# Performance work log

Measured on AMD Instinct MI355X. Metric: run time of the kernel, lower is better.

The kernel has to match this reference:

```python
import jax, jax.numpy as jnp
import numpy as np

GROUPS = 32
GN_EPS = 1e-6
LN_EPS = 1e-5
HEADS = 8
DH = 40


def group_norm(x, w, b):
    # x: [B, C, H, W], GroupNorm over (C//GROUPS, H, W) within each group
    B, C, H, W = x.shape
    xg = x.reshape(B, GROUPS, C // GROUPS, H, W)
    mu = xg.mean(axis=(2, 3, 4), keepdims=True)
    var = xg.var(axis=(2, 3, 4), keepdims=True)
    xg = (xg - mu) * jax.lax.rsqrt(var + GN_EPS)
    return xg.reshape(B, C, H, W) * w[None, :, None, None] + b[None, :, None, None]


def layer_norm(x, w, b):
    mu = x.mean(axis=-1, keepdims=True)
    var = x.var(axis=-1, keepdims=True)
    return (x - mu) * jax.lax.rsqrt(var + LN_EPS) * w + b


def attention(x, ctx, wq, wk, wv, wo, bo):
    # x: [B, N, D], ctx: [B, M, Dc]; weights stored (in, out)
    B, N, _ = x.shape
    M = ctx.shape[1]
    q = (x @ wq).reshape(B, N, HEADS, DH)
    k = (ctx @ wk).reshape(B, M, HEADS, DH)
    v = (ctx @ wv).reshape(B, M, HEADS, DH)
    sim = jnp.einsum('bihd,bjhd->bhij', q, k) * (DH ** -0.5)
    attn = jax.nn.softmax(sim, axis=-1)
    out = jnp.einsum('bhij,bjhd->bihd', attn, v).reshape(B, N, HEADS * DH)
    return out @ wo + bo


def geglu_ff(x, w1, b1, w2, b2):
    h = x @ w1 + b1
    a, g = jnp.split(h, 2, axis=-1)
    return (a * jax.nn.gelu(g, approximate=False)) @ w2 + b2


def conv1x1(x, w, b):
    # w: [C_out, C_in]
    return jnp.einsum('bihw,oi->bohw', x, w) + b[None, :, None, None]


def reference(x, context, gn_w, gn_b, pin_w, pin_b,
              ln1_w, ln1_b, q1, k1, v1, o1_w, o1_b,
              ln2_w, ln2_b, q2, k2, v2, o2_w, o2_b,
              ln3_w, ln3_b, ff1_w, ff1_b, ff2_w, ff2_b,
              pout_w, pout_b):
    B, C, H, W = x.shape
    x_in = x
    h = group_norm(x, gn_w, gn_b)
    h = conv1x1(h, pin_w, pin_b)
    h = h.reshape(B, C, H * W).transpose(0, 2, 1)  # b (h w) c
    # BasicTransformerBlock
    h = attention(layer_norm(h, ln1_w, ln1_b), layer_norm(h, ln1_w, ln1_b), q1, k1, v1, o1_w, o1_b) + h
    h = attention(layer_norm(h, ln2_w, ln2_b), context, q2, k2, v2, o2_w, o2_b) + h
    h = geglu_ff(layer_norm(h, ln3_w, ln3_b), ff1_w, ff1_b, ff2_w, ff2_b) + h
    h = h.transpose(0, 2, 1).reshape(B, C, H, W)
    h = conv1x1(h, pout_w, pout_b)
    return h + x_in


def setup_inputs() -> dict:
    key = jax.random.key(0)
    ks = jax.random.split(key, 20)
    B, C, H, W = 1, 320, 64, 64
    CTX_N, CTX_D = 77, 768
    INNER, FFI = 320, 1280

    def n(k, shape, s=0.02):
        return jax.random.normal(k, shape, jnp.float32) * s

    return {
        'x': jax.random.normal(ks[0], (B, C, H, W), jnp.float32),
        'context': jax.random.normal(ks[1], (B, CTX_N, CTX_D), jnp.float32),
        'gn_w': jnp.ones((C,), jnp.float32), 'gn_b': jnp.zeros((C,), jnp.float32),
        'pin_w': n(ks[2], (INNER, C)), 'pin_b': jnp.zeros((INNER,), jnp.float32),
        'ln1_w': jnp.ones((INNER,), jnp.float32), 'ln1_b': jnp.zeros((INNER,), jnp.float32),
        'q1': n(ks[3], (INNER, INNER)), 'k1': n(ks[4], (INNER, INNER)), 'v1': n(ks[5], (INNER, INNER)),
        'o1_w': n(ks[6], (INNER, INNER)), 'o1_b': jnp.zeros((INNER,), jnp.float32),
        'ln2_w': jnp.ones((INNER,), jnp.float32), 'ln2_b': jnp.zeros((INNER,), jnp.float32),
        'q2': n(ks[7], (INNER, INNER)), 'k2': n(ks[8], (CTX_D, INNER)), 'v2': n(ks[9], (CTX_D, INNER)),
        'o2_w': n(ks[10], (INNER, INNER)), 'o2_b': jnp.zeros((INNER,), jnp.float32),
        'ln3_w': jnp.ones((INNER,), jnp.float32), 'ln3_b': jnp.zeros((INNER,), jnp.float32),
        'ff1_w': n(ks[11], (INNER, 2 * FFI)), 'ff1_b': jnp.zeros((2 * FFI,), jnp.float32),
        'ff2_w': n(ks[12], (FFI, INNER)), 'ff2_b': jnp.zeros((INNER,), jnp.float32),
        'pout_w': n(ks[13], (C, INNER)), 'pout_b': jnp.zeros((C,), jnp.float32),
    }
```

## Files before the change

kernel.cpp:

```cpp
#include <hip/hip_runtime.h>
#include <hip/hip_bf16.h>
#include <math.h>

#define N_SEQ  4096
#define DMODEL 320
#define NHEADS 8
#define DHEAD  40
#define CTXN   77
#define CTXD   768
#define FFI    1280

typedef short s8v __attribute__((ext_vector_type(8)));
typedef short s4v __attribute__((ext_vector_type(4)));
typedef float f4v __attribute__((ext_vector_type(4)));
typedef unsigned short u16;

static __device__ __forceinline__ u16 bf16u(float x) {
    unsigned u = __float_as_uint(x);
    return (u16)((u + 0x7FFFu + ((u >> 16) & 1u)) >> 16);
}
static __device__ __forceinline__ float b2f(u16 v) { return __uint_as_float((unsigned)v << 16); }
static __device__ __forceinline__ unsigned pack2(float a, float b) {
    return (unsigned)bf16u(a) | ((unsigned)bf16u(b) << 16);
}

struct WC { const float* s; u16* d; int K, O, trans; };
struct WCs { WC a[12]; };
__global__ __launch_bounds__(256) void wcast2_k(WCs P) {
    __shared__ float tile[32][33];
    WC w = P.a[blockIdx.y];
    if (w.trans) {
        int ntk = w.K >> 5, nto = w.O >> 5;
        int tid = blockIdx.x;
        if (tid >= ntk * nto) return;
        int tk = tid % ntk, to = tid / ntk;
        int lr = threadIdx.x >> 5, lc = threadIdx.x & 31;
#pragma unroll
        for (int p = 0; p < 4; ++p) {
            int k = tk * 32 + p * 8 + lr;
            tile[p * 8 + lr][lc] = w.s[(size_t)k * w.O + to * 32 + lc];
        }
        __syncthreads();
#pragma unroll
        for (int p = 0; p < 4; ++p) {
            int o = to * 32 + p * 8 + lr;
            w.d[(size_t)o * w.K + tk * 32 + lc] = bf16u(tile[lc][p * 8 + lr]);
        }
    } else {
        int nel = w.K * w.O;
        for (int e = blockIdx.x * 256 + threadIdx.x; e < nel; e += gridDim.x * 256)
            w.d[e] = bf16u(w.s[e]);
    }
}

__global__ __launch_bounds__(256) void gn_stats_k(const float* __restrict__ x,
                                                  const float* __restrict__ gw, const float* __restrict__ gb,
                                                  float* __restrict__ sc, float* __restrict__ sh) {
    __shared__ float red[512];
    __shared__ float ms[2];
    int g = blockIdx.x, t = threadIdx.x;
    const float* xp = x + (size_t)g * 40960;
    float s = 0.f, ss = 0.f;
    for (int i = t; i < 40960; i += 256) { float v = xp[i]; s += v; ss += v * v; }
    red[t] = s; red[256 + t] = ss;
    __syncthreads();
    for (int st = 128; st > 0; st >>= 1) {
        if (t < st) { red[t] += red[t + st]; red[256 + t] += red[256 + t + st]; }
        __syncthreads();
    }
    if (t == 0) {
        float mean = red[0] / 40960.f;
        float var  = red[256] / 40960.f - mean * mean;
        ms[0] = mean; ms[1] = rsqrtf(var + 1e-6f);
    }
    __syncthreads();
    if (t < 10) {
        int c = g * 10 + t;
        float scv = gw[c] * ms[1];
        sc[c] = scv;
        sh[c] = gb[c] - ms[0] * scv;
    }
}

__global__ __launch_bounds__(256) void ln_stats_k(const float* __restrict__ in,
                                                  float* __restrict__ mu, float* __restrict__ rs) {
    int row = blockIdx.x * 4 + (threadIdx.x >> 6), l = threadIdx.x & 63;
    const float* p = in + (size_t)row * DMODEL;
    float s = 0.f, ss = 0.f;
#pragma unroll
    for (int j = 0; j < 5; ++j) { float v = p[l + 64 * j]; s += v; ss += v * v; }
    for (int o = 32; o > 0; o >>= 1) { s += __shfl_xor(s, o); ss += __shfl_xor(ss, o); }
    if (l == 0) {
        float mean = s * (1.f / 320.f);
        float var  = ss * (1.f / 320.f) - mean * mean;
        mu[row] = mean;
        rs[row] = rsqrtf(var + 1e-5f);
    }
}

struct GArg { const u16* Wt; const float* bias; float* outf; u16* outb; int ob_mode; };
#define GP 72
#define QSCALE 0.22811012f

template<int SITE>
__global__ __launch_bounds__(256) void gemm_t(const void* __restrict__ Av, int a_mode, int lda,
                                              const float* __restrict__ mu, const float* __restrict__ rs,
                                              const float* __restrict__ cw, const float* __restrict__ cb,
                                              GArg g0, GArg g1, GArg g2,
                                              const float* __restrict__ res,
                                              int Mrows, int K, int Oout, int obT_stride) {
    __shared__ __align__(16) u16 As[2][64 * GP];
    __shared__ __align__(16) u16 Wsm[2][64 * GP];
    const int t = threadIdx.x;
    const int w = t >> 6, lane = t & 63, c = lane & 15, quad = lane >> 4;
    const int o0 = blockIdx.x * 64, n0 = blockIdx.y * 64;
    GArg g = (blockIdx.z == 0) ? g0 : ((blockIdx.z == 1) ? g1 : g2);
    const f4v zero = {0.f, 0.f, 0.f, 0.f};
    f4v acc[4] = {zero, zero, zero, zero};
    const s8v z8 = {0, 0, 0, 0, 0, 0, 0, 0};
    const int nk = K >> 6;

    float fA[16];
    s8v bA0 = z8, bA1 = z8;
    s8v wv0, wv1;

    auto loadW = [&](int k0) {
        int i0 = t, i1 = t + 256;
        wv0 = *(const s8v*)(g.Wt + (size_t)(o0 + (i0 >> 3)) * K + k0 + (i0 & 7) * 8);
        wv1 = *(const s8v*)(g.Wt + (size_t)(o0 + (i1 >> 3)) * K + k0 + (i1 & 7) * 8);
    };
    auto storeW = [&](int b) {
        int i0 = t, i1 = t + 256;
        *(s8v*)&Wsm[b][(i0 >> 3) * GP + (i0 & 7) * 8] = wv0;
        *(s8v*)&Wsm[b][(i1 >> 3) * GP + (i1 & 7) * 8] = wv1;
    };
    auto loadA = [&](int k0) {
        if (a_mode == 0) {
            const u16* A = (const u16*)Av;
            int i0 = t, i1 = t + 256;
            int nA = n0 + (i0 >> 3), nB = n0 + (i1 >> 3);
            bA0 = (nA < Mrows) ? *(const s8v*)(A + (size_t)nA * lda + k0 + (i0 & 7) * 8) : z8;
            bA1 = (nB < Mrows) ? *(const s8v*)(A + (size_t)nB * lda + k0 + (i1 & 7) * 8) : z8;
        } else if (a_mode == 1) {
            const float* A = (const float*)Av;
            int r = t >> 2, s16 = (t & 3) * 16;
            int n = n0 + r;
            if (n < Mrows) {
                const float* src = A + (size_t)n * lda + k0 + s16;
#pragma unroll
                for (int i = 0; i < 16; ++i) fA[i] = src[i];
            } else {
#pragma unroll
                for (int i = 0; i < 16; ++i) fA[i] = 0.f;
            }
        } else if (a_mode == 2) {
            const float* A = (const float*)Av;
#pragma unroll
            for (int j = 0; j < 16; ++j) {
                int e = t + 256 * j; int nn = e & 63, kk = e >> 6;
                int n = n0 + nn, kgl = k0 + kk;
                fA[j] = (n < Mrows) ? A[(size_t)kgl * lda + n] * cw[kgl] + cb[kgl] : 0.f;
            }
        } else if (a_mode == 3) {
            const float* A = (const float*)Av;
            int r = t >> 2, s16 = (t & 3) * 16;
            int n = n0 + r;
            if (n < Mrows) {
                const float* src = A + (size_t)n * lda + k0 + s16;
                const float* cwp = cw + k0 + s16;
                const float* cbp = cb + k0 + s16;
                float m_ = mu[n], rr = rs[n];
#pragma unroll
                for (int i = 0; i < 16; ++i) fA[i] = (src[i] - m_) * rr * cwp[i] + cbp[i];
            } else {
#pragma unroll
                for (int i = 0; i < 16; ++i) fA[i] = 0.f;
            }
        } else {
            const u16* Op = (const u16*)Av;
            const float* lp = mu;
            int r = t >> 2, s16 = (t & 3) * 16;
            int n = n0 + r;
            int ch0 = k0 + s16;
            int hdA = ch0 / 40;
            int hdB = (ch0 + 15) / 40;
            float invA = 1.f / (lp[(size_t)hdA * N_SEQ + n] + lp[(size_t)(8 + hdA) * N_SEQ + n]);
            float invB = (hdB == hdA) ? invA
                       : 1.f / (lp[(size_t)hdB * N_SEQ + n] + lp[(size_t)(8 + hdB) * N_SEQ + n]);
#pragma unroll
            for (int i = 0; i < 16; ++i) {
                int ch = ch0 + i;
                int hd = ch / 40;
                int d  = ch - hd * 40;
                float num = b2f(Op[((size_t)hd * N_SEQ + n) * DHEAD + d])
                          + b2f(Op[((size_t)(8 + hd) * N_SEQ + n) * DHEAD + d]);
                fA[i] = num * ((hd == hdA) ? invA : invB);
            }
        }
    };
    auto storeA = [&](int b) {
        if (a_mode == 0) {
            int i0 = t, i1 = t + 256;
            *(s8v*)&As[b][(i0 >> 3) * GP + (i0 & 7) * 8] = bA0;
            *(s8v*)&As[b][(i1 >> 3) * GP + (i1 & 7) * 8] = bA1;
        } else if (a_mode == 2) {
#pragma unroll
            for (int j = 0; j < 16; ++j) {
                int e = t + 256 * j; int nn = e & 63, kk = e >> 6;
                As[b][nn * GP + kk] = bf16u(fA[j]);
            }
        } else {
            int r = t >> 2, s16 = (t & 3) * 16;
            unsigned* dst = (unsigned*)&As[b][r * GP + s16];
#pragma unroll
            for (int i = 0; i < 8; ++i) dst[i] = pack2(fA[2 * i], fA[2 * i + 1]);
        }
    };

    loadA(0); loadW(0);
    storeA(0); storeW(0);
    __syncthreads();
    for (int k = 0; k < nk; ++k) {
        const int cur = k & 1;
        if (k + 1 < nk) { loadA((k + 1) << 6); loadW((k + 1) << 6); }
        s8v a0 = *(const s8v*)&As[cur][(w * 16 + c) * GP + quad * 8];
        s8v a1 = *(const s8v*)&As[cur][(w * 16 + c) * GP + 32 + quad * 8];
#pragma unroll
        for (int nt = 0; nt < 4; ++nt) {
            s8v b0 = *(const s8v*)&Wsm[cur][(nt * 16 + c) * GP + quad * 8];
            s8v b1 = *(const s8v*)&Wsm[cur][(nt * 16 + c) * GP + 32 + quad * 8];
            acc[nt] = __builtin_amdgcn_mfma_f32_16x16x32_bf16(a0, b0, acc[nt], 0, 0, 0);
            acc[nt] = __builtin_amdgcn_mfma_f32_16x16x32_bf16(a1, b1, acc[nt], 0, 0, 0);
        }
        if (k + 1 < nk) { storeA(1 - cur); storeW(1 - cur); }
        __syncthreads();
    }
#pragma unroll
    for (int nt = 0; nt < 4; ++nt) {
        int o = o0 + nt * 16 + c;
        float vv[4];
#pragma unroll
        for (int r = 0; r < 4; ++r) vv[r] = acc[nt][r] + (g.bias ? g.bias[o] : 0.f);
        if (g.ob_mode == 3) {
            int nb = n0 + w * 16 + quad * 4;
            const float4 x4 = *(const float4*)(res + (size_t)o * obT_stride + nb);
            float4 o4 = make_float4(vv[0] + x4.x, vv[1] + x4.y, vv[2] + x4.z, vv[3] + x4.w);
            *(float4*)(g.outf + (size_t)o * obT_stride + nb) = o4;
        } else if (g.ob_mode == 4) {
#pragma unroll
            for (int r = 0; r < 4; ++r) {
                int n = n0 + w * 16 + quad * 4 + r;
                float vvv = vv[r];
                if (o < 320) vvv *= QSCALE;
                u16 bv = bf16u(vvv);
                if (o < 320)      g0.outb[(size_t)n * 320 + o] = bv;
                else if (o < 640) g1.outb[(size_t)n * 320 + (o - 320)] = bv;
                else              g2.outb[(size_t)(o - 640) * obT_stride + n] = bv;
            }
        } else {
#pragma unroll
            for (int r = 0; r < 4; ++r) {
                int n = n0 + w * 16 + quad * 4 + r;
                if (n >= Mrows) continue;
                float v = vv[r];
                if (res) v += res[(size_t)n * Oout + o];
                if (g.outf) g.outf[(size_t)n * Oout + o] = v;
                if (g.ob_mode == 1) g.outb[(size_t)n * Oout + o] = bf16u(v);
                else if (g.ob_mode == 2) g.outb[(size_t)o * obT_stride + n] = bf16u(v);
            }
        }
    }
}

__global__ __launch_bounds__(256) void gemm_gg(const float* __restrict__ A, int lda,
                                               const float* __restrict__ mu, const float* __restrict__ rs,
                                               const float* __restrict__ cw, const float* __restrict__ cb,
                                               const u16* __restrict__ Wt, const float* __restrict__ bias,
                                               u16* __restrict__ outb,
                                               int K, int Oout, int geglu_off) {
    __shared__ __align__(16) u16 As[64 * GP];
    __shared__ __align__(16) u16 Wsm[64 * GP];
    __shared__ __align__(16) u16 Wgm[64 * GP];
    const int t = threadIdx.x;
    const int w = t >> 6, lane = t & 63, c = lane & 15, quad = lane >> 4;
    const int o0 = blockIdx.x * 64, n0 = blockIdx.y * 64;
    const f4v zero = {0.f, 0.f, 0.f, 0.f};
    f4v acc[4]  = {zero, zero, zero, zero};
    f4v accg[4] = {zero, zero, zero, zero};
    const int nk = K >> 6;

    float fA[16];
    s8v wv0, wv1, gv0, gv1;

    auto loadWG = [&](int k0) {
        int i0 = t, i1 = t + 256;
        wv0 = *(const s8v*)(Wt + (size_t)(o0 + (i0 >> 3)) * K + k0 + (i0 & 7) * 8);
        wv1 = *(const s8v*)(Wt + (size_t)(o0 + (i1 >> 3)) * K + k0 + (i1 & 7) * 8);
        gv0 = *(const s8v*)(Wt + (size_t)(o0 + (i0 >> 3) + geglu_off) * K + k0 + (i0 & 7) * 8);
        gv1 = *(const s8v*)(Wt + (size_t)(o0 + (i1 >> 3) + geglu_off) * K + k0 + (i1 & 7) * 8);
    };
    auto storeWG = [&]() {
        int i0 = t, i1 = t + 256;
        *(s8v*)&Wsm[(i0 >> 3) * GP + (i0 & 7) * 8] = wv0;
        *(s8v*)&Wsm[(i1 >> 3) * GP + (i1 & 7) * 8] = wv1;
        *(s8v*)&Wgm[(i0 >> 3) * GP + (i0 & 7) * 8] = gv0;
        *(s8v*)&Wgm[(i1 >> 3) * GP + (i1 & 7) * 8] = gv1;
    };
    auto loadA = [&](int k0) {
        int r = t >> 2, s16 = (t & 3) * 16;
        int n = n0 + r;
        const float* src = A + (size_t)n * lda + k0 + s16;
        const float* cwp = cw + k0 + s16;
        const float* cbp = cb + k0 + s16;
        float m_ = mu[n], rr = rs[n];
#pragma unroll
        for (int i = 0; i < 16; ++i) fA[i] = (src[i] - m_) * rr * cwp[i] + cbp[i];
    };
    auto storeA = [&]() {
        int r = t >> 2, s16 = (t & 3) * 16;
        unsigned* dst = (unsigned*)&As[r * GP + s16];
#pragma unroll
        for (int i = 0; i < 8; ++i) dst[i] = pack2(fA[2 * i], fA[2 * i + 1]);
    };

    loadA(0); loadWG(0);
    storeA(); storeWG();
    __syncthreads();
    for (int k = 0; k < nk; ++k) {
        if (k + 1 < nk) { loadA((k + 1) << 6); loadWG((k + 1) << 6); }
        s8v a0 = *(const s8v*)&As[(w * 16 + c) * GP + quad * 8];
        s8v a1 = *(const s8v*)&As[(w * 16 + c) * GP + 32 + quad * 8];
#pragma unroll
        for (int nt = 0; nt < 4; ++nt) {
            s8v b0 = *(const s8v*)&Wsm[(nt * 16 + c) * GP + quad * 8];
            s8v b1 = *(const s8v*)&Wsm[(nt * 16 + c) * GP + 32 + quad * 8];
            acc[nt] = __builtin_amdgcn_mfma_f32_16x16x32_bf16(a0, b0, acc[nt], 0, 0, 0);
            acc[nt] = __builtin_amdgcn_mfma_f32_16x16x32_bf16(a1, b1, acc[nt], 0, 0, 0);
            s8v q0 = *(const s8v*)&Wgm[(nt * 16 + c) * GP + quad * 8];
            s8v q1 = *(const s8v*)&Wgm[(nt * 16 + c) * GP + 32 + quad * 8];
            accg[nt] = __builtin_amdgcn_mfma_f32_16x16x32_bf16(a0, q0, accg[nt], 0, 0, 0);
            accg[nt] = __builtin_amdgcn_mfma_f32_16x16x32_bf16(a1, q1, accg[nt], 0, 0, 0);
        }
        __syncthreads();
        if (k + 1 < nk) {
            storeA(); storeWG();
            __syncthreads();
        }
    }
#pragma unroll
    for (int nt = 0; nt < 4; ++nt) {
        int o = o0 + nt * 16 + c;
#pragma unroll
        for (int r = 0; r < 4; ++r) {
            int n = n0 + w * 16 + quad * 4 + r;
            float v = acc[nt][r] + bias[o];
            float gg = accg[nt][r] + bias[o + geglu_off];
            v = v * 0.5f * gg * (1.f + erff(gg * 0.70710678118654752f));
            outb[(size_t)n * Oout + o] = bf16u(v);
        }
    }
}

#define KSP 40
#define PSP 140
#define VP  136
__global__ __launch_bounds__(256) void attn_self8_k(const u16* __restrict__ qb, const u16* __restrict__ kb,
                                                    const u16* __restrict__ vt,
                                                    u16* __restrict__ Opart, float* __restrict__ lpart) {
    __shared__ __align__(16) u16 Ks[128 * KSP];
    __shared__ __align__(16) u16 Ps[64 * PSP];
    __shared__ __align__(16) u16 Vs[48 * VP];
    const int t = threadIdx.x;
    const int w = t >> 6, lane = t & 63, c = lane & 15, quad = lane >> 4;
    const int hd = blockIdx.y, ks = blockIdx.z;
    const int q0 = blockIdx.x * 64;
    const f4v zero = {0.f, 0.f, 0.f, 0.f};
    const s8v z8 = {0, 0, 0, 0, 0, 0, 0, 0};

    for (int i = t; i < 8 * VP / 2; i += 256) ((unsigned*)&Vs[40 * VP])[i] = 0u;
    __syncthreads();
    if (t < VP) Vs[40 * VP + t] = (u16)0x3F80;

    const u16* qrow = qb + (size_t)(q0 + w * 16 + c) * DMODEL + hd * DHEAD;
    s8v qa0 = *(const s8v*)(qrow + quad * 8);
    s8v qa1 = z8;
    if (quad == 0) qa1 = *(const s8v*)(qrow + 32);

    const int i0 = t, i1 = t + 256, i2 = t + 512;
    const int r0 = i0 / 5, s0 = i0 - r0 * 5;
    const int r1 = i1 / 5, s1 = i1 - r1 * 5;
    const int r2 = i2 / 5, s2 = i2 - r2 * 5;
    const u16* kq0 = kb + (size_t)(ks * 2048 + r0) * DMODEL + hd * DHEAD + s0 * 8;
    const u16* kq1 = kb + (size_t)(ks * 2048 + r1) * DMODEL + hd * DHEAD + s1 * 8;
    const u16* kq2 = kb + (size_t)(ks * 2048 + (t < 128 ? r2 : r0)) * DMODEL + hd * DHEAD + (t < 128 ? s2 : s0) * 8;
    u16* ksd0 = &Ks[r0 * KSP + s0 * 8];
    u16* ksd1 = &Ks[r1 * KSP + s1 * 8];
    u16* ksd2 = &Ks[(t < 128 ? r2 : r0) * KSP + (t < 128 ? s2 : s0) * 8];
    const int d0 = i0 >> 4, g0v = i0 & 15;
    const int d1 = i1 >> 4, g1v = i1 & 15;
    const int d2 = (t < 128 ? (i2 >> 4) : d0), g2v = (t < 128 ? (i2 & 15) : g0v);
    const u16* vq0 = vt + (size_t)(hd * DHEAD + d0) * N_SEQ + ks * 2048 + g0v * 8;
    const u16* vq1 = vt + (size_t)(hd * DHEAD + d1) * N_SEQ + ks * 2048 + g1v * 8;
    const u16* vq2 = vt + (size_t)(hd * DHEAD + d2) * N_SEQ + ks * 2048 + g2v * 8;
    u16* vsd0 = &Vs[d0 * VP + g0v * 8];
    u16* vsd1 = &Vs[d1 * VP + g1v * 8];
    u16* vsd2 = &Vs[d2 * VP + g2v * 8];
    const size_t kadv = (size_t)128 * DMODEL;

    s8v kA = *(const s8v*)kq0, kB = *(const s8v*)kq1, kC = *(const s8v*)kq2;
    s8v vA = *(const s8v*)vq0, vB = *(const s8v*)vq1, vC = *(const s8v*)vq2;
    kq0 += kadv; kq1 += kadv; kq2 += kadv;
    vq0 += 128;  vq1 += 128;  vq2 += 128;

    f4v o0 = zero, o1 = zero, o2 = zero;

    for (int kt = 0; kt < 16; ++kt) {
        __syncthreads();
        *(s8v*)ksd0 = kA; *(s8v*)ksd1 = kB;
        *(s8v*)vsd0 = vA; *(s8v*)vsd1 = vB;
        if (t < 128) { *(s8v*)ksd2 = kC; *(s8v*)vsd2 = vC; }
        if (kt + 1 < 16) {
            kA = *(const s8v*)kq0; kB = *(const s8v*)kq1;
            vA = *(const s8v*)vq0; vB = *(const s8v*)vq1;
            if (t < 128) { kC = *(const s8v*)kq2; vC = *(const s8v*)vq2; }
            kq0 += kadv; kq1 += kadv; kq2 += kadv;
            vq0 += 128;  vq1 += 128;  vq2 += 128;
        }
        __syncthreads();

        f4v sarr[8];
#pragma unroll
        for (int nt = 0; nt < 8; ++nt) {
            const int kr = nt * 16 + c;
            s8v b0 = *(const s8v*)&Ks[kr * KSP + quad * 8];
            s8v b1 = z8;
            if (quad == 0) b1 = *(const s8v*)&Ks[kr * KSP + 32];
            f4v s = __builtin_amdgcn_mfma_f32_16x16x32_bf16(qa0, b0, zero, 0, 0, 0);
            s = __builtin_amdgcn_mfma_f32_16x16x32_bf16(qa1, b1, s, 0, 0, 0);
            sarr[nt] = s;
        }

        u16* psw = &Ps[(size_t)(w * 16 + quad * 4) * PSP + c];
#pragma unroll
        for (int reg = 0; reg < 8; ++reg) {
            const int colb = (reg >> 2) * 64 + (reg & 3) * 16;
#pragma unroll
            for (int r = 0; r < 4; ++r) {
                float pv = exp2f(sarr[reg][r]);
                psw[r * PSP + colb] = (u16)(__float_as_uint(pv) >> 16);
            }
        }

        const u16* prow = &Ps[(size_t)(w * 16 + c) * PSP];
#pragma unroll
        for (int h2 = 0; h2 < 2; ++h2) {
            s8v pa0, pa1;
            {
                s4v lo = *(const s4v*)(prow + h2 * 64 + quad * 8);
                s4v hi = *(const s4v*)(prow + h2 * 64 + quad * 8 + 4);
                pa0 = (s8v){lo[0], lo[1], lo[2], lo[3], hi[0], hi[1], hi[2], hi[3]};
                s4v lo2 = *(const s4v*)(prow + h2 * 64 + 32 + quad * 8);
                s4v hi2 = *(const s4v*)(prow + h2 * 64 + 32 + quad * 8 + 4);
                pa1 = (s8v){lo2[0], lo2[1], lo2[2], lo2[3], hi2[0], hi2[1], hi2[2], hi2[3]};
            }
            {
                s8v v0 = *(const s8v*)&Vs[(0 * 16 + c) * VP + h2 * 64 + quad * 8];
                s8v v1 = *(const s8v*)&Vs[(0 * 16 + c) * VP + h2 * 64 + 32 + quad * 8];
                o0 = __builtin_amdgcn_mfma_f32_16x16x32_bf16(pa0, v0, o0, 0, 0, 0);
                o0 = __builtin_amdgcn_mfma_f32_16x16x32_bf16(pa1, v1, o0, 0, 0, 0);
            }
            {
                s8v v0 = *(const s8v*)&Vs[(1 * 16 + c) * VP + h2 * 64 + quad * 8];
                s8v v1 = *(const s8v*)&Vs[(1 * 16 + c) * VP + h2 * 64 + 32 + quad * 8];
                o1 = __builtin_amdgcn_mfma_f32_16x16x32_bf16(pa0, v0, o1, 0, 0, 0);
                o1 = __builtin_amdgcn_mfma_f32_16x16x32_bf16(pa1, v1, o1, 0, 0, 0);
            }
            {
                s8v v0 = *(const s8v*)&Vs[(2 * 16 + c) * VP + h2 * 64 + quad * 8];
                s8v v1 = *(const s8v*)&Vs[(2 * 16 + c) * VP + h2 * 64 + 32 + quad * 8];
                o2 = __builtin_amdgcn_mfma_f32_16x16x32_bf16(pa0, v0, o2, 0, 0, 0);
                o2 = __builtin_amdgcn_mfma_f32_16x16x32_bf16(pa1, v1, o2, 0, 0, 0);
            }
        }
    }

    const size_t pb = (size_t)(ks * 8 + hd) * N_SEQ;
#pragma unroll
    for (int r = 0; r < 4; ++r) {
        int q = q0 + w * 16 + quad * 4 + r;
        u16* op = Opart + (pb + q) * DHEAD;
        op[c]      = bf16u(o0[r]);
        op[16 + c] = bf16u(o1[r]);
        if (c < 8) op[32 + c] = bf16u(o2[r]);
        if (c == 8) lpart[pb + q] = o2[r];
    }
}

__global__ __launch_bounds__(256) void attn_cross3_k(const u16* __restrict__ qb,
                                                     const u16* __restrict__ kb,
                                                     const u16* __restrict__ vt,
                                                     u16* __restrict__ outb) {
    __shared__ __align__(16) u16 KsPs[64 * PSP];
    __shared__ __align__(16) u16 Vs[48 * VP];
    const int t = threadIdx.x;
    const int w = t >> 6, lane = t & 63, c = lane & 15, quad = lane >> 4;
    const int hd = blockIdx.y;
    const int q0 = blockIdx.x * 64;
    const float SC2 = 0.15811388300841897f * 1.4426950408889634f;
    const f4v zero = {0.f, 0.f, 0.f, 0.f};
    const s8v z8 = {0, 0, 0, 0, 0, 0, 0, 0};

    for (int i = t; i < 48 * VP / 2; i += 256) ((unsigned*)Vs)[i] = 0u;
    __syncthreads();
    if (t < VP) Vs[40 * VP + t] = (u16)0x3F80;
    for (int i = t; i < 400; i += 256) {
        int d = i / 10, kc = i - d * 10;
        s8v v = *(const s8v*)(vt + (size_t)(hd * DHEAD + d) * 128 + kc * 8);
        if (kc == 9) { v[5] = 0; v[6] = 0; v[7] = 0; }
        *(s8v*)&Vs[d * VP + kc * 8] = v;
    }
    for (int i = t; i < 385; i += 256) {
        int r = i / 5, sg = i - r * 5;
        *(s8v*)&KsPs[r * KSP + sg * 8] = *(const s8v*)(kb + (size_t)r * DMODEL + hd * DHEAD + sg * 8);
    }
    const u16* qrow = qb + (size_t)(q0 + w * 16 + c) * DMODEL + hd * DHEAD;
    s8v qa0 = *(const s8v*)(qrow + quad * 8);
    s8v qa1 = z8;
    if (quad == 0) qa1 = *(const s8v*)(qrow + 32);
    __syncthreads();

    f4v sarr[5];
#pragma unroll
    for (int nt = 0; nt < 5; ++nt) {
        const int kr = nt * 16 + c;
        s8v b0 = *(const s8v*)&KsPs[kr * KSP + quad * 8];
        s8v b1 = z8;
        if (quad == 0) b1 = *(const s8v*)&KsPs[kr * KSP + 32];
        f4v s = __builtin_amdgcn_mfma_f32_16x16x32_bf16(qa0, b0, zero, 0, 0, 0);
        s = __builtin_amdgcn_mfma_f32_16x16x32_bf16(qa1, b1, s, 0, 0, 0);
        sarr[nt] = s;
    }
    __syncthreads();

    u16* psw = &KsPs[(size_t)(w * 16 + quad * 4) * PSP + c];
#pragma unroll
    for (int r = 0; r < 4; ++r) {
        float s4 = (c < 13) ? sarr[4][r] : -1e30f;
        float mx = fmaxf(fmaxf(fmaxf(sarr[0][r], sarr[1][r]), fmaxf(sarr[2][r], sarr[3][r])), s4);
        mx = fmaxf(mx, __shfl_xor(mx, 1));
        mx = fmaxf(mx, __shfl_xor(mx, 2));
        mx = fmaxf(mx, __shfl_xor(mx, 4));
        mx = fmaxf(mx, __shfl_xor(mx, 8));
#pragma unroll
        for (int nt = 0; nt < 4; ++nt)
            psw[r * PSP + nt * 16] = bf16u(exp2f((sarr[nt][r] - mx) * SC2));
        psw[r * PSP + 64] = (c < 13) ? bf16u(exp2f((s4 - mx) * SC2)) : (u16)0;
        psw[r * PSP + 80] = 0;
    }

    const u16* prow = &KsPs[(size_t)(w * 16 + c) * PSP];
    f4v o0 = zero, o1 = zero, o2 = zero;
#pragma unroll
    for (int ch = 0; ch < 3; ++ch) {
        s4v lo = *(const s4v*)(prow + ch * 32 + quad * 8);
        s4v hi = *(const s4v*)(prow + ch * 32 + quad * 8 + 4);
        s8v pa = (s8v){lo[0], lo[1], lo[2], lo[3], hi[0], hi[1], hi[2], hi[3]};
        s8v v0 = *(const s8v*)&Vs[(0 * 16 + c) * VP + ch * 32 + quad * 8];
        o0 = __builtin_amdgcn_mfma_f32_16x16x32_bf16(pa, v0, o0, 0, 0, 0);
        s8v v1 = *(const s8v*)&Vs[(1 * 16 + c) * VP + ch * 32 + quad * 8];
        o1 = __builtin_amdgcn_mfma_f32_16x16x32_bf16(pa, v1, o1, 0, 0, 0);
        s8v v2 = *(const s8v*)&Vs[(2 * 16 + c) * VP + ch * 32 + quad * 8];
        o2 = __builtin_amdgcn_mfma_f32_16x16x32_bf16(pa, v2, o2, 0, 0, 0);
    }

#pragma unroll
    for (int r = 0; r < 4; ++r) {
        float inv = 1.f / __shfl(o2[r], (lane & 48) | 8);
        int q = q0 + w * 16 + quad * 4 + r;
        u16* op = outb + (size_t)q * DMODEL + hd * DHEAD;
        op[c]      = bf16u(o0[r] * inv);
        op[16 + c] = bf16u(o1[r] * inv);
        if (c < 8) op[32 + c] = bf16u(o2[r] * inv);
    }
}

extern "C" void kernel_launch(void* const* d_in, const int* in_sizes, int n_in,
                              void* d_out, int out_size, void* d_ws, size_t ws_size,
                              hipStream_t stream) {
    const float* x      = (const float*)d_in[0];
    const float* ctx    = (const float*)d_in[1];
    const float* gn_w   = (const float*)d_in[2];
    const float* gn_b   = (const float*)d_in[3];
    const float* pin_w  = (const float*)d_in[4];
    const float* pin_b  = (const float*)d_in[5];
    const float* ln1_w  = (const float*)d_in[6];
    const float* ln1_b  = (const float*)d_in[7];
    const float* q1     = (const float*)d_in[8];
    const float* k1     = (const float*)d_in[9];
    const float* v1     = (const float*)d_in[10];
    const float* o1_w   = (const float*)d_in[11];
    const float* o1_b   = (const float*)d_in[12];
    const float* ln2_w  = (const float*)d_in[13];
    const float* ln2_b  = (const float*)d_in[14];
    const float* q2     = (const float*)d_in[15];
    const float* k2     = (const float*)d_in[16];
    const float* v2     = (const float*)d_in[17];
    const float* o2_w   = (const float*)d_in[18];
    const float* o2_b   = (const float*)d_in[19];
    const float* ln3_w  = (const float*)d_in[20];
    const float* ln3_b  = (const float*)d_in[21];
    const float* ff1_w  = (const float*)d_in[22];
    const float* ff1_b  = (const float*)d_in[23];
    const float* ff2_w  = (const float*)d_in[24];
    const float* ff2_b  = (const float*)d_in[25];
    const float* pout_w = (const float*)d_in[26];
    const float* pout_b = (const float*)d_in[27];
    float* out = (float*)d_out;

    char* base = (char*)d_ws;
    float* h     = (float*)(base);
    u16*   qb16  = (u16*)(base + 5242880);
    u16*   kb16  = (u16*)(base + 7864320);
    u16*   vt16  = (u16*)(base + 10485760);
    u16*   ao16  = (u16*)(base + 13107200);
    u16*   ffg16 = (u16*)(base + 5242880);
    u16*   wbase = (u16*)(base + 15728640);
    u16* pinT  = wbase;
    u16* q1T   = pinT  + 102400;
    u16* k1T   = q1T   + 102400;
    u16* v1T   = k1T   + 102400;
    u16* o1T   = v1T   + 102400;
    u16* q2T   = o1T   + 102400;
    u16* o2T   = q2T   + 102400;
    u16* k2T   = o2T   + 102400;
    u16* v2T   = k2T   + 245760;
    u16* ff1T  = v2T   + 245760;
    u16* ff2T  = ff1T  + 819200;
    u16* poutT = ff2T  + 409600;
    float* lnmu = (float*)(base + 20807680);
    float* lnrs = lnmu + 4096;
    u16*   k2b16 = (u16*)(lnrs + 4096);
    u16*   v2t16 = (u16*)(lnrs + 4096 + 25600);
    u16*   Opart = (u16*)(lnrs + 4096 + 51200);
    float* lpart = (float*)(Opart + (size_t)2 * 8 * 4096 * 40);
    float* gnsc  = lpart + 2 * 8 * 4096;
    float* gnsh  = gnsc + 320;

    WCs wd;
    wd.a[0]  = {pin_w,  pinT,  320,  320,  0};
    wd.a[1]  = {q1,     q1T,   320,  320,  1};
    wd.a[2]  = {k1,     k1T,   320,  320,  1};
    wd.a[3]  = {v1,     v1T,   320,  320,  1};
    wd.a[4]  = {o1_w,   o1T,   320,  320,  1};
    wd.a[5]  = {q2,     q2T,   320,  320,  1};
    wd.a[6]  = {o2_w,   o2T,   320,  320,  1};
    wd.a[7]  = {k2,     k2T,   768,  320,  1};
    wd.a[8]  = {v2,     v2T,   768,  320,  1};
    wd.a[9]  = {ff1_w,  ff1T,  320,  2560, 1};
    wd.a[10] = {ff2_w,  ff2T,  1280, 320,  1};
    wd.a[11] = {pout_w, poutT, 320,  320,  0};
    wcast2_k<<<dim3(800, 12), 256, 0, stream>>>(wd);

    GArg gz = {nullptr, nullptr, nullptr, nullptr, 0};

    gn_stats_k<<<32, 256, 0, stream>>>(x, gn_w, gn_b, gnsc, gnsh);
    {
        GArg g0 = {pinT, pin_b, h, nullptr, 0};
        gemm_t<0><<<dim3(5, 64, 1), 256, 0, stream>>>(x, 2, 4096, nullptr, nullptr, gnsc, gnsh,
                                                      g0, gz, gz, nullptr, 4096, 320, 320, 0);
    }
    ln_stats_k<<<1024, 256, 0, stream>>>(h, lnmu, lnrs);
    {
        GArg g0 = {q1T, nullptr, nullptr, qb16, 4};
        GArg g1 = {nullptr, nullptr, nullptr, kb16, 0};
        GArg g2 = {nullptr, nullptr, nullptr, vt16, 0};
        gemm_t<1><<<dim3(15, 64, 1), 256, 0, stream>>>(h, 3, 320, lnmu, lnrs, ln1_w, ln1_b,
                                                       g0, g1, g2, nullptr, 4096, 320, 960, 4096);
    }
    attn_self8_k<<<dim3(64, 8, 2), 256, 0, stream>>>(qb16, kb16, vt16, Opart, lpart);
    {
        GArg g0 = {o1T, o1_b, h, nullptr, 0};
        gemm_t<2><<<dim3(5, 64, 1), 256, 0, stream>>>(Opart, 4, 0, lpart, nullptr, nullptr, nullptr,
                                                      g0, gz, gz, h, 4096, 320, 320, 0);
    }
    ln_stats_k<<<1024, 256, 0, stream>>>(h, lnmu, lnrs);
    {
        GArg g0 = {q2T, nullptr, nullptr, qb16, 1};
        gemm_t<3><<<dim3(5, 64, 1), 256, 0, stream>>>(h, 3, 320, lnmu, lnrs, ln2_w, ln2_b,
                                                      g0, gz, gz, nullptr, 4096, 320, 320, 0);
    }
    {
        GArg g0 = {k2T, nullptr, nullptr, k2b16, 1};
        GArg g1 = {v2T, nullptr, nullptr, v2t16, 2};
        gemm_t<4><<<dim3(5, 2, 2), 256, 0, stream>>>(ctx, 1, 768, nullptr, nullptr, nullptr, nullptr,
                                                     g0, g1, gz, nullptr, 77, 768, 320, 128);
    }
    attn_cross3_k<<<dim3(64, 8), 256, 0, stream>>>(qb16, k2b16, v2t16, ao16);
    {
        GArg g0 = {o2T, o2_b, h, nullptr, 0};
        gemm_t<5><<<dim3(5, 64, 1), 256, 0, stream>>>(ao16, 0, 320, nullptr, nullptr, nullptr, nullptr,
                                                      g0, gz, gz, h, 4096, 320, 320, 0);
    }
    ln_stats_k<<<1024, 256, 0, stream>>>(h, lnmu, lnrs);
    gemm_gg<<<dim3(20, 64, 1), 256, 0, stream>>>(h, 320, lnmu, lnrs, ln3_w, ln3_b,
                                                 ff1T, ff1_b, ffg16, 320, 1280, 1280);
    {
        GArg g0 = {ff2T, ff2_b, h, nullptr, 0};
        gemm_t<6><<<dim3(5, 64, 1), 256, 0, stream>>>(ffg16, 0, 1280, nullptr, nullptr, nullptr, nullptr,
                                                      g0, gz, gz, h, 4096, 1280, 320, 0);
    }
    {
        GArg g0 = {poutT, pout_b, out, nullptr, 3};
        gemm_t<7><<<dim3(5, 64, 1), 256, 0, stream>>>(h, 1, 320, nullptr, nullptr, nullptr, nullptr,
                                                      g0, gz, gz, x, 4096, 320, 320, 4096);
    }
}
```

Before: 439.3 us.

## Load GEMM weight tiles directly into LDS with XOR-swizzled layout

Weight tiles in the templated GEMM now move from global memory straight into shared memory using the global_load_lds builtin. This replaces the path of loading into registers and then storing to LDS. Because that load cannot pad rows, the tile drops its padded stride and uses an XOR swizzle on the 16-byte chunk index to avoid bank conflicts on reads. The aim is to save VGPRs and LDS-store instructions, and to overlap weight fetch with the MFMA work. The risk is a correctness error in the swizzle mapping or in the async-load wait semantics before the __syncthreads.

```diff
diff --git a/kernel.cpp b/kernel.cpp
--- a/kernel.cpp
+++ b/kernel.cpp
@@ -23,6 +23,10 @@
 static __device__ __forceinline__ unsigned pack2(float a, float b) {
     return (unsigned)bf16u(a) | ((unsigned)bf16u(b) << 16);
 }
+
+#define GLD_LDS16(gp, lp) __builtin_amdgcn_global_load_lds( \
+    (const __attribute__((address_space(1))) void*)(gp),    \
+    (__attribute__((address_space(3))) void*)(lp), 16, 0, 0)
 
 struct WC { const float* s; u16* d; int K, O, trans; };
 struct WCs { WC a[12]; };
@@ -110,7 +114,7 @@
                                               const float* __restrict__ res,
                                               int Mrows, int K, int Oout, int obT_stride) {
     __shared__ __align__(16) u16 As[2][64 * GP];
-    __shared__ __align__(16) u16 Wsm[2][64 * GP];
+    __shared__ __align__(16) u16 Wsm[2][64 * 64];
     const int t = threadIdx.x;
     const int w = t >> 6, lane = t & 63, c = lane & 15, quad = lane >> 4;
     const int o0 = blockIdx.x * 64, n0 = blockIdx.y * 64;
@@ -122,17 +126,17 @@
 
     float fA[16];
     s8v bA0 = z8, bA1 = z8;
-    s8v wv0, wv1;
-
-    auto loadW = [&](int k0) {
-        int i0 = t, i1 = t + 256;
-        wv0 = *(const s8v*)(g.Wt + (size_t)(o0 + (i0 >> 3)) * K + k0 + (i0 & 7) * 8);
-        wv1 = *(const s8v*)(g.Wt + (size_t)(o0 + (i1 >> 3)) * K + k0 + (i1 & 7) * 8);
-    };
-    auto storeW = [&](int b) {
-        int i0 = t, i1 = t + 256;
-        *(s8v*)&Wsm[b][(i0 >> 3) * GP + (i0 & 7) * 8] = wv0;
-        *(s8v*)&Wsm[b][(i1 >> 3) * GP + (i1 & 7) * 8] = wv1;
+
+    const u16* gW0 = g.Wt + (size_t)(o0 + w * 16 + (lane >> 3)) * K + ((lane & 7) ^ (lane >> 3)) * 8;
+    const u16* gW1 = gW0 + (size_t)8 * K;
+    const int wdst = w * 1024;
+    const int swb0 = 8 * (quad ^ (c & 7));
+    const int swb1 = 8 * ((quad + 4) ^ (c & 7));
+
+    auto gllW = [&](int b) {
+        GLD_LDS16(gW0, &Wsm[b][wdst]);
+        GLD_LDS16(gW1, &Wsm[b][wdst + 512]);
+        gW0 += 64; gW1 += 64;
     };
     auto loadA = [&](int k0) {
         if (a_mode == 0) {
@@ -217,22 +221,22 @@
         }
     };
 
-    loadA(0); loadW(0);
-    storeA(0); storeW(0);
+    gllW(0); loadA(0);
+    storeA(0);
     __syncthreads();
     for (int k = 0; k < nk; ++k) {
         const int cur = k & 1;
-        if (k + 1 < nk) { loadA((k + 1) << 6); loadW((k + 1) << 6); }
+        if (k + 1 < nk) { gllW(1 - cur); loadA((k + 1) << 6); }
         s8v a0 = *(const s8v*)&As[cur][(w * 16 + c) * GP + quad * 8];
         s8v a1 = *(const s8v*)&As[cur][(w * 16 + c) * GP + 32 + quad * 8];
 #pragma unroll
         for (int nt = 0; nt < 4; ++nt) {
-            s8v b0 = *(const s8v*)&Wsm[cur][(nt * 16 + c) * GP + quad * 8];
-            s8v b1 = *(const s8v*)&Wsm[cur][(nt * 16 + c) * GP + 32 + quad * 8];
+            s8v b0 = *(const s8v*)&Wsm[cur][(nt * 16 + c) * 64 + swb0];
+            s8v b1 = *(const s8v*)&Wsm[cur][(nt * 16 + c) * 64 + swb1];
             acc[nt] = __builtin_amdgcn_mfma_f32_16x16x32_bf16(a0, b0, acc[nt], 0, 0, 0);
             acc[nt] = __builtin_amdgcn_mfma_f32_16x16x32_bf16(a1, b1, acc[nt], 0, 0, 0);
         }
-        if (k + 1 < nk) { storeA(1 - cur); storeW(1 - cur); }
+        if (k + 1 < nk) { storeA(1 - cur); }
         __syncthreads();
     }
 #pragma unroll
```

After: 436.2 us. No clear change (-0.7%).
